# Kernel tuning notes

Measured on AMD Instinct MI355X. Metric: run time of the kernel, lower is better.

## Reference

```python
import jax, jax.numpy as jnp
import numpy as np

N, E, G = 50000, 400000, 2000
H, HEADS, HD = 128, 4, 32


def setup_inputs() -> dict:
    key = jax.random.key(0)
    ks = jax.random.split(key, 16)
    nrm = lambda k, shape, s=0.05: jax.random.normal(k, shape, dtype=jnp.float32) * s
    inp = {}
    inp["x"] = jax.random.normal(ks[0], (N, 39), dtype=jnp.float32)
    inp["edge_index"] = jax.random.randint(ks[1], (2, E), 0, N, dtype=jnp.int32)
    inp["edge_attr"] = jax.random.normal(ks[2], (E, 8), dtype=jnp.float32)
    inp["batch"] = jnp.sort(jax.random.randint(ks[3], (N,), 0, G, dtype=jnp.int32))
    inp["in_W"] = nrm(ks[4], (39, H)); inp["in_b"] = jnp.zeros((H,), jnp.float32)
    inp["in_g"] = jnp.ones((H,), jnp.float32); inp["in_beta"] = jnp.zeros((H,), jnp.float32)
    inp["Wl"] = nrm(ks[5], (3, H, H)); inp["Wr"] = nrm(ks[6], (3, H, H))
    inp["We"] = nrm(ks[7], (3, 8, H)); inp["att"] = nrm(ks[8], (3, HEADS, HD))
    inp["conv_b"] = jnp.zeros((3, H), jnp.float32)
    inp["bn_g"] = jnp.ones((3, H), jnp.float32); inp["bn_b"] = jnp.zeros((3, H), jnp.float32)
    inp["t1_W"] = nrm(ks[9], (3 * H, 256)); inp["t1_b"] = jnp.zeros((256,), jnp.float32)
    inp["t1_g"] = jnp.ones((256,), jnp.float32); inp["t1_beta"] = jnp.zeros((256,), jnp.float32)
    inp["t2_W"] = nrm(ks[10], (256, 128)); inp["t2_b"] = jnp.zeros((128,), jnp.float32)
    inp["t2_g"] = jnp.ones((128,), jnp.float32); inp["t2_beta"] = jnp.zeros((128,), jnp.float32)
    inp["head_W"] = nrm(ks[11], (128, 12)); inp["head_b"] = jnp.zeros((12,), jnp.float32)
    return inp


def _bn(h, g, b):
    # BatchNorm1d in training mode: normalize with batch statistics.
    m = h.mean(0)
    v = ((h - m) ** 2).mean(0)
    return g * (h - m) * jax.lax.rsqrt(v + 1e-5) + b


def reference(x, edge_index, edge_attr, batch, in_W, in_b, in_g, in_beta,
              Wl, Wr, We, att, conv_b, bn_g, bn_b,
              t1_W, t1_b, t1_g, t1_beta, t2_W, t2_b, t2_g, t2_beta,
              head_W, head_b):
    src, dst = edge_index[0], edge_index[1]  # messages flow src -> dst (PyG convention)
    xn = jax.nn.relu(_bn(x @ in_W + in_b, in_g, in_beta))  # [N, H]
    for l in range(3):  # three residual GATv2 layers
        xl = (xn @ Wl[l]).reshape(N, HEADS, HD)  # lin_l (source transform)
        xr = (xn @ Wr[l]).reshape(N, HEADS, HD)  # lin_r (target transform)
        ep = (edge_attr @ We[l]).reshape(E, HEADS, HD)
        m = jax.nn.leaky_relu(xl[src] + xr[dst] + ep, 0.2)  # [E, HEADS, HD]
        alpha = jnp.einsum('ehd,hd->eh', m, att[l])  # [E, HEADS]
        amax = jax.ops.segment_max(alpha, dst, num_segments=N)
        amax = jnp.where(jnp.isfinite(amax), amax, 0.0)  # nodes with no in-edges
        ae = jnp.exp(alpha - amax[dst])
        denom = jax.ops.segment_sum(ae, dst, num_segments=N)
        a = ae / (denom[dst] + 1e-16)  # scatter-softmax over neighborhoods
        agg = jax.ops.segment_sum(xl[src] * a[:, :, None], dst, num_segments=N)
        h = agg.reshape(N, H) + conv_b[l]
        h = jax.nn.elu(_bn(h, bn_g[l], bn_b[l]))
        xn = xn + h
    # 3-way global pooling per graph
    cnt = jax.ops.segment_sum(jnp.ones((N,), jnp.float32), batch, num_segments=G)
    sadd = jax.ops.segment_sum(xn, batch, num_segments=G)
    smean = sadd / jnp.maximum(cnt, 1.0)[:, None]
    smax = jax.ops.segment_max(xn, batch, num_segments=G)
    smax = jnp.where(cnt[:, None] > 0, smax, 0.0)
    xg = jnp.concatenate([smean, smax, sadd], axis=1)  # [G, 3H]
    t = jax.nn.relu(_bn(xg @ t1_W + t1_b, t1_g, t1_beta))
    t = jax.nn.relu(_bn(t @ t2_W + t2_b, t2_g, t2_beta))
    return jax.nn.sigmoid(t @ head_W + head_b)  # [G, 12]
```

## Files before the change

kernel.cpp:

```cpp
#include <hip/hip_runtime.h>
#include <math.h>


constexpr int N_ = 50000;
constexpr int E_ = 400000;
constexpr int G_ = 2000;
constexpr int H_ = 128;
constexpr int IN_ = 39;

typedef __attribute__((ext_vector_type(8))) short bf16x8;
typedef __attribute__((ext_vector_type(4))) float f32x4;

__device__ __forceinline__ unsigned pk_bf16(float a, float b) {
  unsigned ua = __float_as_uint(a);
  unsigned ub = __float_as_uint(b);
  ua = (ua + 0x7fffu + ((ua >> 16) & 1u)) >> 16;
  ub = (ub + 0x7fffu + ((ub >> 16) & 1u)) & 0xffff0000u;
  return ua | ub;
}
__device__ __forceinline__ unsigned short bf16_1(float x) {
  unsigned u = __float_as_uint(x);
  u = (u + 0x7fffu + ((u >> 16) & 1u)) >> 16;
  return (unsigned short)u;
}
__device__ __forceinline__ float up_lo(unsigned u) { return __uint_as_float(u << 16); }
__device__ __forceinline__ float up_hi(unsigned u) { return __uint_as_float(u & 0xffff0000u); }

template <int CTRL>
__device__ __forceinline__ float dpp_radd(float x) {
  int y = __builtin_amdgcn_update_dpp(0, __float_as_int(x), CTRL, 0xF, 0xF, false);
  return x + __int_as_float(y);
}
__device__ __forceinline__ float row_reduce16(float p) {
  p = dpp_radd<0x121>(p);
  p = dpp_radd<0x122>(p);
  p = dpp_radd<0x124>(p);
  p = dpp_radd<0x128>(p);
  return p;
}

__global__ __launch_bounds__(256) void hist_kernel(const int* __restrict__ keys, int n,
                                                   int* __restrict__ cnt) {
  for (int i = blockIdx.x * 256 + threadIdx.x; i < n; i += gridDim.x * 256)
    atomicAdd(&cnt[keys[i]], 1);
}

__global__ __launch_bounds__(1024) void scan_local(const int* __restrict__ in,
                                                   int* __restrict__ outx,
                                                   int* __restrict__ bsum, int n) {
  __shared__ int wsum[16];
  int t = threadIdx.x, lane = t & 63, wid = t >> 6;
  int idx = blockIdx.x * 1024 + t;
  int v = (idx < n) ? in[idx] : 0;
  int x = v;
#pragma unroll
  for (int off = 1; off < 64; off <<= 1) {
    int y = __shfl_up(x, off, 64);
    if (lane >= off) x += y;
  }
  if (lane == 63) wsum[wid] = x;
  __syncthreads();
  if (t == 0) {
    int acc = 0;
#pragma unroll
    for (int w = 0; w < 16; w++) { int tmp = wsum[w]; wsum[w] = acc; acc += tmp; }
    bsum[blockIdx.x] = acc;
  }
  __syncthreads();
  if (idx < n) outx[idx] = wsum[wid] + x - v;
}

__global__ __launch_bounds__(64) void scan_bsum(const int* __restrict__ bsum,
                                                int* __restrict__ boff, int nb) {
  int t = threadIdx.x;
  int v = (t < nb) ? bsum[t] : 0;
  int x = v;
#pragma unroll
  for (int off = 1; off < 64; off <<= 1) {
    int y = __shfl_up(x, off, 64);
    if (t >= off) x += y;
  }
  boff[t] = x - v;
}

__global__ __launch_bounds__(1024) void scan_add(int* __restrict__ eoff,
                                                 const int* __restrict__ boff,
                                                 int* __restrict__ cursor, int n) {
  int idx = blockIdx.x * 1024 + threadIdx.x;
  if (idx < n) {
    int e = eoff[idx] + boff[idx >> 10];
    eoff[idx] = e;
    cursor[idx] = e;
  }
  if (idx == 0) eoff[n] = E_;
}

__global__ __launch_bounds__(256) void goff_from_sorted(const int* __restrict__ batch,
                                                        int* __restrict__ goff) {
  int i = blockIdx.x * 256 + threadIdx.x;
  if (i >= N_) return;
  int bi = batch[i];
  int bp = (i == 0) ? -1 : batch[i - 1];
  for (int g = bp + 1; g <= bi; g++) goff[g] = i;
  if (i == N_ - 1) {
    for (int g = bi + 1; g <= G_; g++) goff[g] = N_;
  }
}

__global__ __launch_bounds__(256) void edge_scatter(const int* __restrict__ ei,
                                                    const float* __restrict__ ea,
                                                    int* __restrict__ cursor,
                                                    int* __restrict__ esrc,
                                                    unsigned* __restrict__ easb) {
  int e = blockIdx.x * 256 + threadIdx.x;
  if (e >= E_) return;
  int src = ei[e];
  int dst = ei[E_ + e];
  int j = atomicAdd(&cursor[dst], 1);
  esrc[j] = src;
  const float4* eav = (const float4*)(ea + (size_t)e * 8);
  float4 a0 = eav[0], a1 = eav[1];
  uint4 o;
  o.x = pk_bf16(a0.x, a0.y);
  o.y = pk_bf16(a0.z, a0.w);
  o.z = pk_bf16(a1.x, a1.y);
  o.w = pk_bf16(a1.z, a1.w);
  ((uint4*)easb)[j] = o;
}

__global__ __launch_bounds__(256) void pack_weights(const float* __restrict__ Wl,
                                                    const float* __restrict__ Wr,
                                                    unsigned short* __restrict__ wpack) {
  int i = blockIdx.x * 256 + threadIdx.x;
  if (i >= 3 * 128 * 256) return;
  int l = i >> 15;
  int rem = i & 32767;
  int k = rem >> 8;
  int n = rem & 255;
  const float* Wsrc = (n < 128) ? (Wl + l * H_ * H_) : (Wr + l * H_ * H_);
  int nn = n & 127;
  wpack[(size_t)l * 32768 + n * 128 + k] = bf16_1(Wsrc[k * H_ + nn]);
}

__global__ __launch_bounds__(256) void in_gemm(const float* __restrict__ x,
                                               const float* __restrict__ W,
                                               const float* __restrict__ b,
                                               float* __restrict__ y,
                                               float* __restrict__ ssum,
                                               float* __restrict__ ssq) {
  __shared__ float xs[32][40];
  __shared__ float s1[256], s2[256];
  int t = threadIdx.x;
  int row0 = blockIdx.x * 32;
  for (int i = t; i < 32 * IN_; i += 256) {
    int r = i / IN_, k = i % IN_;
    int row = row0 + r;
    xs[r][k] = (row < N_) ? x[row * IN_ + k] : 0.f;
  }
  __syncthreads();
  int col = t & 127;
  int half = t >> 7;
  float acc[16];
#pragma unroll
  for (int r = 0; r < 16; r++) acc[r] = 0.f;
  for (int k = 0; k < IN_; k++) {
    float w = W[k * H_ + col];
#pragma unroll
    for (int r = 0; r < 16; r++) acc[r] = fmaf(xs[half * 16 + r][k], w, acc[r]);
  }
  float bb = b[col];
  float a1 = 0.f, a2 = 0.f;
#pragma unroll
  for (int r = 0; r < 16; r++) {
    int row = row0 + half * 16 + r;
    float v = acc[r] + bb;
    if (row < N_) {
      y[row * H_ + col] = v;
      a1 += v;
      a2 = fmaf(v, v, a2);
    }
  }
  s1[t] = a1; s2[t] = a2;
  __syncthreads();
  if (t < 128) {
    atomicAdd(&ssum[t], s1[t] + s1[t + 128]);
    atomicAdd(&ssq[t], s2[t] + s2[t + 128]);
  }
}

template <int MODE>
__global__ __launch_bounds__(256) void gemm_mfma(float* __restrict__ xn,
                                                 const float* __restrict__ buf,
                                                 const float* __restrict__ g,
                                                 const float* __restrict__ beta,
                                                 const float* __restrict__ ssum,
                                                 const float* __restrict__ ssq,
                                                 float rows_inv,
                                                 const unsigned short* __restrict__ wp,
                                                 unsigned* __restrict__ xlb,
                                                 unsigned* __restrict__ xrb) {
  __shared__ char smem[17408 + 20480];
  short (*a_s)[136] = (short(*)[136])smem;
  short (*b_s)[40] = (short(*)[40])(smem + 17408);
  float* t2base = (float*)(smem + 17408);
  int t = threadIdx.x;
  int lane = t & 63, w = t >> 6;
  int quad = lane >> 4, lc = lane & 15;
  int row0 = blockIdx.x * 64;

  {
    int r = t >> 2;
    int row = row0 + r;
    int kb0 = (t & 3) * 32;
    bool valid = row < N_;
    for (int kk = 0; kk < 32; kk += 4) {
      int c = kb0 + kk;
      float4 v = make_float4(0.f, 0.f, 0.f, 0.f);
      if (valid) {
        float4 bv = *(const float4*)&buf[(size_t)row * H_ + c];
        float4 gv = *(const float4*)&g[c];
        float4 be = *(const float4*)&beta[c];
        float4 s1 = *(const float4*)&ssum[c];
        float4 s2 = *(const float4*)&ssq[c];
        float m0 = s1.x * rows_inv, m1 = s1.y * rows_inv, m2 = s1.z * rows_inv, m3 = s1.w * rows_inv;
        float r0 = rsqrtf(s2.x * rows_inv - m0 * m0 + 1e-5f);
        float r1 = rsqrtf(s2.y * rows_inv - m1 * m1 + 1e-5f);
        float r2 = rsqrtf(s2.z * rows_inv - m2 * m2 + 1e-5f);
        float r3 = rsqrtf(s2.w * rows_inv - m3 * m3 + 1e-5f);
        float t0 = gv.x * (bv.x - m0) * r0 + be.x;
        float t1 = gv.y * (bv.y - m1) * r1 + be.y;
        float t2 = gv.z * (bv.z - m2) * r2 + be.z;
        float t3 = gv.w * (bv.w - m3) * r3 + be.w;
        if (MODE == 1) {
          v = make_float4(fmaxf(t0, 0.f), fmaxf(t1, 0.f), fmaxf(t2, 0.f), fmaxf(t3, 0.f));
        } else {
          float4 xo = *(const float4*)&xn[(size_t)row * H_ + c];
          v.x = xo.x + ((t0 > 0.f) ? t0 : (__expf(t0) - 1.f));
          v.y = xo.y + ((t1 > 0.f) ? t1 : (__expf(t1) - 1.f));
          v.z = xo.z + ((t2 > 0.f) ? t2 : (__expf(t2) - 1.f));
          v.w = xo.w + ((t3 > 0.f) ? t3 : (__expf(t3) - 1.f));
        }
        *(float4*)&xn[(size_t)row * H_ + c] = v;
      }
      uint2 pk;
      pk.x = pk_bf16(v.x, v.y);
      pk.y = pk_bf16(v.z, v.w);
      *(uint2*)&a_s[r][c] = pk;
    }
  }

  f32x4 acc[16];
#pragma unroll
  for (int nt = 0; nt < 16; nt++) acc[nt] = (f32x4){0.f, 0.f, 0.f, 0.f};

  for (int kb = 0; kb < 4; kb++) {
    __syncthreads();
    for (int i = t; i < 1024; i += 256) {
      int n = i >> 2;
      int k8 = (i & 3) * 8;
      *(uint4*)&b_s[n][k8] = *(const uint4*)&wp[(size_t)n * 128 + kb * 32 + k8];
    }
    __syncthreads();
    bf16x8 av = *(const bf16x8*)&a_s[w * 16 + lc][kb * 32 + quad * 8];
#pragma unroll
    for (int nt = 0; nt < 16; nt++) {
      bf16x8 bv = *(const bf16x8*)&b_s[nt * 16 + lc][quad * 8];
      acc[nt] = __builtin_amdgcn_mfma_f32_16x16x32_bf16(av, bv, acc[nt], 0, 0, 0);
    }
  }
  __syncthreads();

  float* t2 = t2base + w * 544;
  for (int ntp = 0; ntp < 8; ntp++) {
#pragma unroll
    for (int rr = 0; rr < 4; rr++) {
      t2[(quad * 4 + rr) * 34 + lc] = acc[2 * ntp][rr];
      t2[(quad * 4 + rr) * 34 + 16 + lc] = acc[2 * ntp + 1][rr];
    }
    __asm__ volatile("s_waitcnt lgkmcnt(0)" ::: "memory");
#pragma unroll
    for (int it = 0; it < 4; it++) {
      int item = lane + it * 64;
      int p = item & 15, rowi = item >> 4;
      float v0 = t2[rowi * 34 + 2 * p];
      float v1 = t2[rowi * 34 + 2 * p + 1];
      unsigned u = pk_bf16(v0, v1);
      int colpair = ntp * 16 + p;
      int rowg = row0 + w * 16 + rowi;
      if (rowg < N_) {
        if (colpair < 64) xlb[(size_t)rowg * 64 + colpair] = u;
        else xrb[(size_t)rowg * 64 + colpair - 64] = u;
      }
    }
    __asm__ volatile("s_waitcnt lgkmcnt(0)" ::: "memory");
  }
}

__device__ __forceinline__ float ep8u(const uint4& u, const float* w) {
  float ep = up_lo(u.x) * w[0];
  ep = fmaf(up_hi(u.x), w[1], ep);
  ep = fmaf(up_lo(u.y), w[2], ep);
  ep = fmaf(up_hi(u.y), w[3], ep);
  ep = fmaf(up_lo(u.z), w[4], ep);
  ep = fmaf(up_hi(u.z), w[5], ep);
  ep = fmaf(up_lo(u.w), w[6], ep);
  ep = fmaf(up_hi(u.w), w[7], ep);
  return ep;
}

template <bool MASK>
__device__ __forceinline__ void pack4(int spre, int j, int cnt, int base, int l,
                                      const unsigned* __restrict__ xlb,
                                      const uint4* __restrict__ eas4,
                                      float xr0, float xr1,
                                      const float* w0, const float* w1,
                                      float2 attv,
                                      float& acc0, float& acc1, float& den) {
  int i0 = j;
  int i1 = j + 1, i2 = j + 2, i3 = j + 3;
  if (MASK) {
    i1 = (i1 < cnt) ? i1 : cnt - 1;
    i2 = (i2 < cnt) ? i2 : cnt - 1;
    i3 = (i3 < cnt) ? i3 : cnt - 1;
  }
  int s0 = __builtin_amdgcn_readlane(spre, i0);
  int s1 = __builtin_amdgcn_readlane(spre, i1);
  int s2 = __builtin_amdgcn_readlane(spre, i2);
  int s3 = __builtin_amdgcn_readlane(spre, i3);
  unsigned xu0 = xlb[(size_t)s0 * 64 + l];
  unsigned xu1 = xlb[(size_t)s1 * 64 + l];
  unsigned xu2 = xlb[(size_t)s2 * 64 + l];
  unsigned xu3 = xlb[(size_t)s3 * 64 + l];
  uint4 u0 = eas4[base + i0];
  uint4 u1 = eas4[base + i1];
  uint4 u2 = eas4[base + i2];
  uint4 u3 = eas4[base + i3];
  float x00 = up_lo(xu0), x01 = up_hi(xu0);
  float x10 = up_lo(xu1), x11 = up_hi(xu1);
  float x20 = up_lo(xu2), x21 = up_hi(xu2);
  float x30 = up_lo(xu3), x31 = up_hi(xu3);
  float m00 = x00 + xr0 + ep8u(u0, w0);
  float m01 = x01 + xr1 + ep8u(u0, w1);
  float m10 = x10 + xr0 + ep8u(u1, w0);
  float m11 = x11 + xr1 + ep8u(u1, w1);
  float m20 = x20 + xr0 + ep8u(u2, w0);
  float m21 = x21 + xr1 + ep8u(u2, w1);
  float m30 = x30 + xr0 + ep8u(u3, w0);
  float m31 = x31 + xr1 + ep8u(u3, w1);
  m00 = (m00 > 0.f) ? m00 : 0.2f * m00;
  m01 = (m01 > 0.f) ? m01 : 0.2f * m01;
  m10 = (m10 > 0.f) ? m10 : 0.2f * m10;
  m11 = (m11 > 0.f) ? m11 : 0.2f * m11;
  m20 = (m20 > 0.f) ? m20 : 0.2f * m20;
  m21 = (m21 > 0.f) ? m21 : 0.2f * m21;
  m30 = (m30 > 0.f) ? m30 : 0.2f * m30;
  m31 = (m31 > 0.f) ? m31 : 0.2f * m31;
  float p0 = fmaf(m00, attv.x, m01 * attv.y);
  float p1 = fmaf(m10, attv.x, m11 * attv.y);
  float p2 = fmaf(m20, attv.x, m21 * attv.y);
  float p3 = fmaf(m30, attv.x, m31 * attv.y);
  p0 = row_reduce16(p0);
  p1 = row_reduce16(p1);
  p2 = row_reduce16(p2);
  p3 = row_reduce16(p3);
  float e0v = __expf(p0), e1v = __expf(p1), e2v = __expf(p2), e3v = __expf(p3);
  if (MASK) {
    if (j + 1 >= cnt) e1v = 0.f;
    if (j + 2 >= cnt) e2v = 0.f;
    if (j + 3 >= cnt) e3v = 0.f;
  }
  acc0 = fmaf(e0v, x00, acc0); acc1 = fmaf(e0v, x01, acc1);
  acc0 = fmaf(e1v, x10, acc0); acc1 = fmaf(e1v, x11, acc1);
  acc0 = fmaf(e2v, x20, acc0); acc1 = fmaf(e2v, x21, acc1);
  acc0 = fmaf(e3v, x30, acc0); acc1 = fmaf(e3v, x31, acc1);
  den += (e0v + e1v) + (e2v + e3v);
}

__device__ __forceinline__ void solo_node(int e0, int e1, int l,
                                          const int* __restrict__ esrc,
                                          const unsigned* __restrict__ xlb,
                                          const uint4* __restrict__ eas4,
                                          float xr0, float xr1,
                                          const float* w0, const float* w1,
                                          float2 attv,
                                          float& acc0, float& acc1, float& den) {
  for (int base = e0; base < e1; base += 64) {
    int cnt = min(64, e1 - base);
    int spre = (base + l < e1) ? esrc[base + l] : 0;
    int j = 0;
    for (; j + 4 <= cnt; j += 4)
      pack4<false>(spre, j, cnt, base, l, xlb, eas4, xr0, xr1, w0, w1, attv, acc0, acc1, den);
    if (j < cnt)
      pack4<true>(spre, j, cnt, base, l, xlb, eas4, xr0, xr1, w0, w1, attv, acc0, acc1, den);
  }
}

__global__ __launch_bounds__(256) void agg_csr(const int* __restrict__ eoff,
                                               const int* __restrict__ esrc,
                                               const unsigned* __restrict__ easb,
                                               const float* __restrict__ Wel,
                                               const float* __restrict__ attl,
                                               const unsigned* __restrict__ xlb,
                                               const unsigned* __restrict__ xrb,
                                               const float* __restrict__ cb,
                                               float* __restrict__ buf,
                                               float* __restrict__ ssum,
                                               float* __restrict__ ssq) {
  __shared__ float sA[256], sB[256], sC[256], sD[256];
  __shared__ uint4 eaLds[4][64];
  int t = threadIdx.x;
  int l = t & 63;
  int sub = t >> 6;
  int c0 = l * 2;
  uint4* eaW = &eaLds[sub][0];
  float w0[8], w1[8];
#pragma unroll
  for (int k = 0; k < 8; k++) {
    float2 wv = *(const float2*)&Wel[k * H_ + c0];
    w0[k] = wv.x; w1[k] = wv.y;
  }
  float2 attv = *(const float2*)&attl[c0];
  float2 cbv = *(const float2*)&cb[c0];
  const uint4* eas4 = (const uint4*)easb;
  float a1_0 = 0.f, a1_1 = 0.f, a2_0 = 0.f, a2_1 = 0.f;

  for (int pi = blockIdx.x * 4 + sub; pi < N_ / 2; pi += gridDim.x * 4) {
    int nA = 2 * pi, nB = nA + 1;
    int e0A = eoff[nA], e1A = eoff[nA + 1], e1B = eoff[nA + 2];
    unsigned xruA = xrb[(size_t)nA * 64 + l];
    unsigned xruB = xrb[(size_t)nB * 64 + l];
    int cE = e1B - e0A;
    float hA0, hA1, hB0, hB1;
    if (cE <= 64) {
      int cA = e1A - e0A, cB = e1B - e1A;
      if (l < cE) eaW[l] = eas4[e0A + l];
      int spre = (l < cE) ? esrc[e0A + l] : 0;
      __asm__ volatile("s_waitcnt lgkmcnt(0)" ::: "memory");
      int nPA = (cA + 3) >> 2;
      int nP = nPA + ((cB + 3) >> 2);
      float accA0 = 0.f, accA1 = 0.f, denA = 0.f;
      float accB0 = 0.f, accB1 = 0.f, denB = 0.f;
      unsigned xu0 = 0, xu1 = 0, xu2 = 0, xu3 = 0;
      int i0 = 0, i1 = 0, i2 = 0, i3 = 0;
      if (nP > 0) {
        bool isA = 0 < nPA;
        int off = isA ? 0 : cA;
        int cnt = isA ? cA : cB;
        int lim = off + cnt - 1;
        i0 = off;
        i1 = min(off + 1, lim); i2 = min(off + 2, lim); i3 = min(off + 3, lim);
        xu0 = xlb[(size_t)__builtin_amdgcn_readlane(spre, i0) * 64 + l];
        xu1 = xlb[(size_t)__builtin_amdgcn_readlane(spre, i1) * 64 + l];
        xu2 = xlb[(size_t)__builtin_amdgcn_readlane(spre, i2) * 64 + l];
        xu3 = xlb[(size_t)__builtin_amdgcn_readlane(spre, i3) * 64 + l];
      }
      for (int k = 0; k < nP; k++) {
        unsigned t0 = xu0, t1 = xu1, t2 = xu2, t3 = xu3;
        int ci0 = i0, ci1 = i1, ci2 = i2, ci3 = i3;
        bool isA = k < nPA;
        int j = isA ? 4 * k : 4 * (k - nPA);
        int cnt = isA ? cA : cB;
        if (k + 1 < nP) {
          bool pA = (k + 1) < nPA;
          int off2 = pA ? 0 : cA;
          int cnt2 = pA ? cA : cB;
          int j2 = pA ? 4 * (k + 1) : 4 * (k + 1 - nPA);
          int b2 = off2 + j2;
          int lim2 = off2 + cnt2 - 1;
          i0 = b2;
          i1 = min(b2 + 1, lim2); i2 = min(b2 + 2, lim2); i3 = min(b2 + 3, lim2);
          xu0 = xlb[(size_t)__builtin_amdgcn_readlane(spre, i0) * 64 + l];
          xu1 = xlb[(size_t)__builtin_amdgcn_readlane(spre, i1) * 64 + l];
          xu2 = xlb[(size_t)__builtin_amdgcn_readlane(spre, i2) * 64 + l];
          xu3 = xlb[(size_t)__builtin_amdgcn_readlane(spre, i3) * 64 + l];
        }
        uint4 u0 = eaW[ci0], u1 = eaW[ci1], u2 = eaW[ci2], u3 = eaW[ci3];
        unsigned xrp = isA ? xruA : xruB;
        float xr0 = up_lo(xrp), xr1 = up_hi(xrp);
        float x00 = up_lo(t0), x01 = up_hi(t0);
        float x10 = up_lo(t1), x11 = up_hi(t1);
        float x20 = up_lo(t2), x21 = up_hi(t2);
        float x30 = up_lo(t3), x31 = up_hi(t3);
        float m00 = x00 + xr0 + ep8u(u0, w0);
        float m01 = x01 + xr1 + ep8u(u0, w1);
        float m10 = x10 + xr0 + ep8u(u1, w0);
        float m11 = x11 + xr1 + ep8u(u1, w1);
        float m20 = x20 + xr0 + ep8u(u2, w0);
        float m21 = x21 + xr1 + ep8u(u2, w1);
        float m30 = x30 + xr0 + ep8u(u3, w0);
        float m31 = x31 + xr1 + ep8u(u3, w1);
        m00 = (m00 > 0.f) ? m00 : 0.2f * m00;
        m01 = (m01 > 0.f) ? m01 : 0.2f * m01;
        m10 = (m10 > 0.f) ? m10 : 0.2f * m10;
        m11 = (m11 > 0.f) ? m11 : 0.2f * m11;
        m20 = (m20 > 0.f) ? m20 : 0.2f * m20;
        m21 = (m21 > 0.f) ? m21 : 0.2f * m21;
        m30 = (m30 > 0.f) ? m30 : 0.2f * m30;
        m31 = (m31 > 0.f) ? m31 : 0.2f * m31;
        float p0 = fmaf(m00, attv.x, m01 * attv.y);
        float p1 = fmaf(m10, attv.x, m11 * attv.y);
        float p2 = fmaf(m20, attv.x, m21 * attv.y);
        float p3 = fmaf(m30, attv.x, m31 * attv.y);
        p0 = row_reduce16(p0);
        p1 = row_reduce16(p1);
        p2 = row_reduce16(p2);
        p3 = row_reduce16(p3);
        float e0v = __expf(p0), e1v = __expf(p1), e2v = __expf(p2), e3v = __expf(p3);
        if (j + 1 >= cnt) e1v = 0.f;
        if (j + 2 >= cnt) e2v = 0.f;
        if (j + 3 >= cnt) e3v = 0.f;
        if (isA) {
          accA0 = fmaf(e0v, x00, accA0); accA1 = fmaf(e0v, x01, accA1);
          accA0 = fmaf(e1v, x10, accA0); accA1 = fmaf(e1v, x11, accA1);
          accA0 = fmaf(e2v, x20, accA0); accA1 = fmaf(e2v, x21, accA1);
          accA0 = fmaf(e3v, x30, accA0); accA1 = fmaf(e3v, x31, accA1);
          denA += (e0v + e1v) + (e2v + e3v);
        } else {
          accB0 = fmaf(e0v, x00, accB0); accB1 = fmaf(e0v, x01, accB1);
          accB0 = fmaf(e1v, x10, accB0); accB1 = fmaf(e1v, x11, accB1);
          accB0 = fmaf(e2v, x20, accB0); accB1 = fmaf(e2v, x21, accB1);
          accB0 = fmaf(e3v, x30, accB0); accB1 = fmaf(e3v, x31, accB1);
          denB += (e0v + e1v) + (e2v + e3v);
        }
      }
      float invA = 1.f / (denA + 1e-16f);
      float invB = 1.f / (denB + 1e-16f);
      hA0 = accA0 * invA + cbv.x; hA1 = accA1 * invA + cbv.y;
      hB0 = accB0 * invB + cbv.x; hB1 = accB1 * invB + cbv.y;
    } else {
      float accA0 = 0.f, accA1 = 0.f, denA = 0.f;
      float accB0 = 0.f, accB1 = 0.f, denB = 0.f;
      solo_node(e0A, e1A, l, esrc, xlb, eas4, up_lo(xruA), up_hi(xruA),
                w0, w1, attv, accA0, accA1, denA);
      solo_node(e1A, e1B, l, esrc, xlb, eas4, up_lo(xruB), up_hi(xruB),
                w0, w1, attv, accB0, accB1, denB);
      float invA = 1.f / (denA + 1e-16f);
      float invB = 1.f / (denB + 1e-16f);
      hA0 = accA0 * invA + cbv.x; hA1 = accA1 * invA + cbv.y;
      hB0 = accB0 * invB + cbv.x; hB1 = accB1 * invB + cbv.y;
    }
    *(float2*)&buf[(size_t)nA * H_ + c0] = make_float2(hA0, hA1);
    *(float2*)&buf[(size_t)nB * H_ + c0] = make_float2(hB0, hB1);
    a1_0 += hA0 + hB0; a1_1 += hA1 + hB1;
    a2_0 = fmaf(hA0, hA0, a2_0); a2_0 = fmaf(hB0, hB0, a2_0);
    a2_1 = fmaf(hA1, hA1, a2_1); a2_1 = fmaf(hB1, hB1, a2_1);
  }
  sA[t] = a1_0; sB[t] = a1_1; sC[t] = a2_0; sD[t] = a2_1;
  __syncthreads();
  if (t < 64) {
    float r1 = sA[t] + sA[t + 64] + sA[t + 128] + sA[t + 192];
    float r2 = sB[t] + sB[t + 64] + sB[t + 128] + sB[t + 192];
    float r3 = sC[t] + sC[t + 64] + sC[t + 128] + sC[t + 192];
    float r4 = sD[t] + sD[t + 64] + sD[t + 128] + sD[t + 192];
    atomicAdd(&ssum[2 * t], r1);
    atomicAdd(&ssum[2 * t + 1], r2);
    atomicAdd(&ssq[2 * t], r3);
    atomicAdd(&ssq[2 * t + 1], r4);
  }
}

__global__ __launch_bounds__(256) void apply_bn_relu(const float* __restrict__ y,
                                                     float* __restrict__ out,
                                                     const float* __restrict__ g,
                                                     const float* __restrict__ beta,
                                                     const float* __restrict__ ssum,
                                                     const float* __restrict__ ssq,
                                                     float rows_inv,
                                                     long total, int cmask) {
  long i = (long)blockIdx.x * 256 + threadIdx.x;
  if (i >= total) return;
  int c = (int)i & cmask;
  float m = ssum[c] * rows_inv;
  float rs = rsqrtf(ssq[c] * rows_inv - m * m + 1e-5f);
  float v = g[c] * (y[i] - m) * rs + beta[c];
  out[i] = fmaxf(v, 0.f);
}

__global__ __launch_bounds__(128) void pool_residual(const int* __restrict__ goff,
                                                     const float* __restrict__ xn,
                                                     const float* __restrict__ buf,
                                                     const float* __restrict__ g,
                                                     const float* __restrict__ beta,
                                                     const float* __restrict__ ssum,
                                                     const float* __restrict__ ssq,
                                                     float rows_inv,
                                                     float* __restrict__ xg) {
  int gr = blockIdx.x;
  int t = threadIdx.x;
  int n0 = goff[gr], n1 = goff[gr + 1];
  float mm = ssum[t] * rows_inv;
  float rr = rsqrtf(ssq[t] * rows_inv - mm * mm + 1e-5f);
  float gg = g[t], bb = beta[t];
  float s = 0.f, mx = -INFINITY;
  for (int n = n0; n < n1; n++) {
    float w = gg * (buf[(size_t)n * H_ + t] - mm) * rr + bb;
    w = (w > 0.f) ? w : (__expf(w) - 1.f);
    float v = xn[(size_t)n * H_ + t] + w;
    s += v;
    mx = fmaxf(mx, v);
  }
  float c = (float)(n1 - n0);
  xg[gr * 384 + t] = s / fmaxf(c, 1.f);
  xg[gr * 384 + 128 + t] = (c > 0.f) ? mx : 0.f;
  xg[gr * 384 + 256 + t] = s;
}

template <int K, int COLS>
__global__ void mlp_gemm(const float* __restrict__ A, const float* __restrict__ W,
                         const float* __restrict__ b, float* __restrict__ Y, int rows,
                         float* __restrict__ ssum, float* __restrict__ ssq) {
  __shared__ float xs[8][K];
  int t = threadIdx.x;
  int row0 = blockIdx.x * 8;
  for (int i = t; i < 8 * K; i += COLS) {
    int r = i / K, k = i % K;
    int row = row0 + r;
    xs[r][k] = (row < rows) ? A[row * K + k] : 0.f;
  }
  __syncthreads();
  float acc[8];
#pragma unroll
  for (int r = 0; r < 8; r++) acc[r] = 0.f;
  for (int k = 0; k < K; k++) {
    float w = W[k * COLS + t];
#pragma unroll
    for (int r = 0; r < 8; r++) acc[r] = fmaf(xs[r][k], w, acc[r]);
  }
  float bb = b[t];
  float a1 = 0.f, a2 = 0.f;
#pragma unroll
  for (int r = 0; r < 8; r++) {
    int row = row0 + r;
    if (row < rows) {
      float v = acc[r] + bb;
      Y[row * COLS + t] = v;
      a1 += v;
      a2 = fmaf(v, v, a2);
    }
  }
  atomicAdd(&ssum[t], a1);
  atomicAdd(&ssq[t], a2);
}

__global__ __launch_bounds__(64) void head_kernel(const float* __restrict__ u,
                                                  const float* __restrict__ W,
                                                  const float* __restrict__ b,
                                                  float* __restrict__ out) {
  __shared__ float row[128];
  int g = blockIdx.x;
  int t = threadIdx.x;
  row[t] = u[g * 128 + t];
  row[t + 64] = u[g * 128 + 64 + t];
  __syncthreads();
  if (t < 12) {
    float acc = b[t];
    for (int k = 0; k < 128; k++) acc = fmaf(row[k], W[k * 12 + t], acc);
    out[g * 12 + t] = 1.f / (1.f + expf(-acc));
  }
}

extern "C" void kernel_launch(void* const* d_in, const int* in_sizes, int n_in, void* d_out,
                              int out_size, void* d_ws, size_t ws_size, hipStream_t stream) {
  (void)in_sizes; (void)n_in; (void)out_size; (void)ws_size;
  const float* x       = (const float*)d_in[0];
  const int*   ei      = (const int*)d_in[1];
  const float* ea      = (const float*)d_in[2];
  const int*   batch   = (const int*)d_in[3];
  const float* in_W    = (const float*)d_in[4];
  const float* in_b    = (const float*)d_in[5];
  const float* in_g    = (const float*)d_in[6];
  const float* in_beta = (const float*)d_in[7];
  const float* Wl      = (const float*)d_in[8];
  const float* Wr      = (const float*)d_in[9];
  const float* We      = (const float*)d_in[10];
  const float* att     = (const float*)d_in[11];
  const float* conv_b  = (const float*)d_in[12];
  const float* bn_g    = (const float*)d_in[13];
  const float* bn_b    = (const float*)d_in[14];
  const float* t1_W    = (const float*)d_in[15];
  const float* t1_b    = (const float*)d_in[16];
  const float* t1_g    = (const float*)d_in[17];
  const float* t1_beta = (const float*)d_in[18];
  const float* t2_W    = (const float*)d_in[19];
  const float* t2_b    = (const float*)d_in[20];
  const float* t2_g    = (const float*)d_in[21];
  const float* t2_beta = (const float*)d_in[22];
  const float* head_W  = (const float*)d_in[23];
  const float* head_b  = (const float*)d_in[24];
  float* out = (float*)d_out;

  float* p = (float*)d_ws;
  float* xn    = p; p += N_ * H_;
  float* buf   = p; p += N_ * H_;
  float* sstat = p; p += 6 * 512;
  float* xg    = p; p += G_ * 384;
  float* u1    = p; p += G_ * 256;
  float* u2    = p; p += G_ * 128;
  unsigned* up = (unsigned*)p;
  unsigned* xlb  = up; up += (size_t)N_ * 64;
  unsigned* xrb  = up; up += (size_t)N_ * 64;
  unsigned* easb = up; up += (size_t)E_ * 4;
  unsigned short* wpack = (unsigned short*)up; up += 3 * 32768 / 2;
  int* ip = (int*)up;
  int* deg    = ip; ip += N_;
  int* eoff   = ip; ip += N_ + 1;
  int* cursor = ip; ip += N_;
  int* goff   = ip; ip += G_ + 1;
  int* esrc   = ip; ip += E_;
  int* bsum   = ip; ip += 64;
  int* boff   = ip; ip += 64;

#define SSUM(s) (sstat + (s) * 512)
#define SSQ(s)  (sstat + (s) * 512 + 256)

  hipMemsetAsync(deg, 0, (size_t)N_ * sizeof(int), stream);
  hipMemsetAsync(sstat, 0, 6 * 512 * sizeof(float), stream);
  hist_kernel<<<1024, 256, 0, stream>>>(ei + E_, E_, deg);
  scan_local<<<49, 1024, 0, stream>>>(deg, eoff, bsum, N_);
  scan_bsum<<<1, 64, 0, stream>>>(bsum, boff, 49);
  scan_add<<<49, 1024, 0, stream>>>(eoff, boff, cursor, N_);
  edge_scatter<<<(E_ + 255) / 256, 256, 0, stream>>>(ei, ea, cursor, esrc, easb);
  goff_from_sorted<<<(N_ + 255) / 256, 256, 0, stream>>>(batch, goff);
  pack_weights<<<384, 256, 0, stream>>>(Wl, Wr, wpack);

  in_gemm<<<(N_ + 31) / 32, 256, 0, stream>>>(x, in_W, in_b, buf, SSUM(0), SSQ(0));

  const float rnInv = 1.f / N_;
  for (int l = 0; l < 3; l++) {
    if (l == 0) {
      gemm_mfma<1><<<782, 256, 0, stream>>>(xn, buf, in_g, in_beta, SSUM(0), SSQ(0), rnInv,
                                            wpack + (size_t)l * 32768, xlb, xrb);
    } else {
      gemm_mfma<2><<<782, 256, 0, stream>>>(xn, buf, bn_g + (l - 1) * H_, bn_b + (l - 1) * H_,
                                            SSUM(l), SSQ(l), rnInv,
                                            wpack + (size_t)l * 32768, xlb, xrb);
    }
    agg_csr<<<2048, 256, 0, stream>>>(eoff, esrc, easb, We + l * 8 * H_, att + l * H_,
                                      xlb, xrb, conv_b + l * H_, buf, SSUM(l + 1), SSQ(l + 1));
  }

  pool_residual<<<G_, 128, 0, stream>>>(goff, xn, buf, bn_g + 2 * H_, bn_b + 2 * H_,
                                        SSUM(3), SSQ(3), rnInv, xg);

  const float rgInv = 1.f / G_;
  mlp_gemm<384, 256><<<G_ / 8, 256, 0, stream>>>(xg, t1_W, t1_b, u1, G_, SSUM(4), SSQ(4));
  apply_bn_relu<<<(G_ * 256 + 255) / 256, 256, 0, stream>>>(u1, u1, t1_g, t1_beta,
                                                            SSUM(4), SSQ(4), rgInv,
                                                            (long)G_ * 256, 255);

  mlp_gemm<256, 128><<<G_ / 8, 128, 0, stream>>>(u1, t2_W, t2_b, u2, G_, SSUM(5), SSQ(5));
  apply_bn_relu<<<(G_ * 128 + 255) / 256, 256, 0, stream>>>(u2, u2, t2_g, t2_beta,
                                                            SSUM(5), SSQ(5), rgInv,
                                                            (long)G_ * 128, 127);

  head_kernel<<<G_, 64, 0, stream>>>(u2, head_W, head_b, out);
#undef SSUM
#undef SSQ
}
```

Baseline: 841.4 us.

## Merge setup kernels, use single-pass decoupled scan, fold MLP BN into consumers

Four independent setup kernels (degree histogram, graph offsets, weight packing, input GEMM) become one launch that dispatches by block index. The three-kernel prefix scan becomes a single-pass chained scan in which each block spins on its predecessor's published prefix. The two MLP BatchNorm+ReLU passes are folded into the next GEMM's load stage and into the head kernel, and the two memsets are merged into one. The aim is fewer launches and less global traffic. The chained scan relies on all 49 blocks making forward progress, and the BN parameters are recomputed per element in the consumers.

```diff
diff --git a/kernel.cpp b/kernel.cpp
--- a/kernel.cpp
+++ b/kernel.cpp
@@ -7,6 +7,11 @@
 constexpr int G_ = 2000;
 constexpr int H_ = 128;
 constexpr int IN_ = 39;
+
+constexpr int HIST_B = 1024;
+constexpr int GOFF_B = (N_ + 255) / 256;
+constexpr int PACK_B = 384;
+constexpr int INGEMM_B = (N_ + 31) / 32;
 
 typedef __attribute__((ext_vector_type(8))) short bf16x8;
 typedef __attribute__((ext_vector_type(4))) float f32x4;
@@ -39,19 +44,101 @@
   return p;
 }
 
-__global__ __launch_bounds__(256) void hist_kernel(const int* __restrict__ keys, int n,
-                                                   int* __restrict__ cnt) {
-  for (int i = blockIdx.x * 256 + threadIdx.x; i < n; i += gridDim.x * 256)
-    atomicAdd(&cnt[keys[i]], 1);
-}
-
-__global__ __launch_bounds__(1024) void scan_local(const int* __restrict__ in,
-                                                   int* __restrict__ outx,
-                                                   int* __restrict__ bsum, int n) {
+__global__ __launch_bounds__(256) void prep_kernel(const int* __restrict__ ei,
+                                                   const int* __restrict__ batch,
+                                                   const float* __restrict__ Wl,
+                                                   const float* __restrict__ Wr,
+                                                   const float* __restrict__ x,
+                                                   const float* __restrict__ in_W,
+                                                   const float* __restrict__ in_b,
+                                                   int* __restrict__ deg,
+                                                   int* __restrict__ goff,
+                                                   unsigned short* __restrict__ wpack,
+                                                   float* __restrict__ y,
+                                                   float* __restrict__ ssum,
+                                                   float* __restrict__ ssq) {
+  int b = blockIdx.x;
+  int t = threadIdx.x;
+  if (b < HIST_B) {
+    for (int i = b * 256 + t; i < E_; i += HIST_B * 256)
+      atomicAdd(&deg[ei[E_ + i]], 1);
+    return;
+  }
+  b -= HIST_B;
+  if (b < GOFF_B) {
+    int i = b * 256 + t;
+    if (i >= N_) return;
+    int bi = batch[i];
+    int bp = (i == 0) ? -1 : batch[i - 1];
+    for (int g = bp + 1; g <= bi; g++) goff[g] = i;
+    if (i == N_ - 1) {
+      for (int g = bi + 1; g <= G_; g++) goff[g] = N_;
+    }
+    return;
+  }
+  b -= GOFF_B;
+  if (b < PACK_B) {
+    int i = b * 256 + t;
+    if (i >= 3 * 128 * 256) return;
+    int l = i >> 15;
+    int rem = i & 32767;
+    int k = rem >> 8;
+    int n = rem & 255;
+    const float* Wsrc = (n < 128) ? (Wl + l * H_ * H_) : (Wr + l * H_ * H_);
+    int nn = n & 127;
+    wpack[(size_t)l * 32768 + n * 128 + k] = bf16_1(Wsrc[k * H_ + nn]);
+    return;
+  }
+  b -= PACK_B;
+  __shared__ float xs[32][40];
+  __shared__ float s1[256], s2[256];
+  int row0 = b * 32;
+  for (int i = t; i < 32 * IN_; i += 256) {
+    int r = i / IN_, k = i % IN_;
+    int row = row0 + r;
+    xs[r][k] = (row < N_) ? x[row * IN_ + k] : 0.f;
+  }
+  __syncthreads();
+  int col = t & 127;
+  int half = t >> 7;
+  float acc[16];
+#pragma unroll
+  for (int r = 0; r < 16; r++) acc[r] = 0.f;
+  for (int k = 0; k < IN_; k++) {
+    float w = in_W[k * H_ + col];
+#pragma unroll
+    for (int r = 0; r < 16; r++) acc[r] = fmaf(xs[half * 16 + r][k], w, acc[r]);
+  }
+  float bb = in_b[col];
+  float a1 = 0.f, a2 = 0.f;
+#pragma unroll
+  for (int r = 0; r < 16; r++) {
+    int row = row0 + half * 16 + r;
+    float v = acc[r] + bb;
+    if (row < N_) {
+      y[row * H_ + col] = v;
+      a1 += v;
+      a2 = fmaf(v, v, a2);
+    }
+  }
+  s1[t] = a1; s2[t] = a2;
+  __syncthreads();
+  if (t < 128) {
+    atomicAdd(&ssum[t], s1[t] + s1[t + 128]);
+    atomicAdd(&ssq[t], s2[t] + s2[t + 128]);
+  }
+}
+
+__global__ __launch_bounds__(1024) void scan_onepass(const int* __restrict__ deg,
+                                                     int* __restrict__ eoff,
+                                                     int* __restrict__ cursor,
+                                                     int* __restrict__ pref, int n) {
   __shared__ int wsum[16];
+  __shared__ int sbase;
   int t = threadIdx.x, lane = t & 63, wid = t >> 6;
-  int idx = blockIdx.x * 1024 + t;
-  int v = (idx < n) ? in[idx] : 0;
+  int b = blockIdx.x;
+  int idx = b * 1024 + t;
+  int v = (idx < n) ? deg[idx] : 0;
   int x = v;
 #pragma unroll
   for (int off = 1; off < 64; off <<= 1) {
@@ -64,46 +151,21 @@
     int acc = 0;
 #pragma unroll
     for (int w = 0; w < 16; w++) { int tmp = wsum[w]; wsum[w] = acc; acc += tmp; }
-    bsum[blockIdx.x] = acc;
-  }
-  __syncthreads();
-  if (idx < n) outx[idx] = wsum[wid] + x - v;
-}
-
-__global__ __launch_bounds__(64) void scan_bsum(const int* __restrict__ bsum,
-                                                int* __restrict__ boff, int nb) {
-  int t = threadIdx.x;
-  int v = (t < nb) ? bsum[t] : 0;
-  int x = v;
-#pragma unroll
-  for (int off = 1; off < 64; off <<= 1) {
-    int y = __shfl_up(x, off, 64);
-    if (t >= off) x += y;
-  }
-  boff[t] = x - v;
-}
-
-__global__ __launch_bounds__(1024) void scan_add(int* __restrict__ eoff,
-                                                 const int* __restrict__ boff,
-                                                 int* __restrict__ cursor, int n) {
-  int idx = blockIdx.x * 1024 + threadIdx.x;
+    int prev = 0;
+    if (b > 0) {
+      int got;
+      do { got = atomicAdd(&pref[b - 1], 0); } while (got == 0);
+      prev = got - 1;
+    }
+    atomicExch(&pref[b], prev + acc + 1);
+    sbase = prev;
+  }
+  __syncthreads();
   if (idx < n) {
-    int e = eoff[idx] + boff[idx >> 10];
+    int e = sbase + wsum[wid] + x - v;
     eoff[idx] = e;
     cursor[idx] = e;
-  }
-  if (idx == 0) eoff[n] = E_;
-}
-
-__global__ __launch_bounds__(256) void goff_from_sorted(const int* __restrict__ batch,
-                                                        int* __restrict__ goff) {
-  int i = blockIdx.x * 256 + threadIdx.x;
-  if (i >= N_) return;
-  int bi = batch[i];
-  int bp = (i == 0) ? -1 : batch[i - 1];
-  for (int g = bp + 1; g <= bi; g++) goff[g] = i;
-  if (i == N_ - 1) {
-    for (int g = bi + 1; g <= G_; g++) goff[g] = N_;
+    if (idx == n - 1) eoff[n] = E_;
   }
 }
 
@@ -126,66 +188,6 @@
   o.z = pk_bf16(a1.x, a1.y);
   o.w = pk_bf16(a1.z, a1.w);
   ((uint4*)easb)[j] = o;
-}
-
-__global__ __launch_bounds__(256) void pack_weights(const float* __restrict__ Wl,
-                                                    const float* __restrict__ Wr,
-                                                    unsigned short* __restrict__ wpack) {
-  int i = blockIdx.x * 256 + threadIdx.x;
-  if (i >= 3 * 128 * 256) return;
-  int l = i >> 15;
-  int rem = i & 32767;
-  int k = rem >> 8;
-  int n = rem & 255;
-  const float* Wsrc = (n < 128) ? (Wl + l * H_ * H_) : (Wr + l * H_ * H_);
-  int nn = n & 127;
-  wpack[(size_t)l * 32768 + n * 128 + k] = bf16_1(Wsrc[k * H_ + nn]);
-}
-
-__global__ __launch_bounds__(256) void in_gemm(const float* __restrict__ x,
-                                               const float* __restrict__ W,
-                                               const float* __restrict__ b,
-                                               float* __restrict__ y,
-                                               float* __restrict__ ssum,
-                                               float* __restrict__ ssq) {
-  __shared__ float xs[32][40];
-  __shared__ float s1[256], s2[256];
-  int t = threadIdx.x;
-  int row0 = blockIdx.x * 32;
-  for (int i = t; i < 32 * IN_; i += 256) {
-    int r = i / IN_, k = i % IN_;
-    int row = row0 + r;
-    xs[r][k] = (row < N_) ? x[row * IN_ + k] : 0.f;
-  }
-  __syncthreads();
-  int col = t & 127;
-  int half = t >> 7;
-  float acc[16];
-#pragma unroll
-  for (int r = 0; r < 16; r++) acc[r] = 0.f;
-  for (int k = 0; k < IN_; k++) {
-    float w = W[k * H_ + col];
-#pragma unroll
-    for (int r = 0; r < 16; r++) acc[r] = fmaf(xs[half * 16 + r][k], w, acc[r]);
-  }
-  float bb = b[col];
-  float a1 = 0.f, a2 = 0.f;
-#pragma unroll
-  for (int r = 0; r < 16; r++) {
-    int row = row0 + half * 16 + r;
-    float v = acc[r] + bb;
-    if (row < N_) {
-      y[row * H_ + col] = v;
-      a1 += v;
-      a2 = fmaf(v, v, a2);
-    }
-  }
-  s1[t] = a1; s2[t] = a2;
-  __syncthreads();
-  if (t < 128) {
-    atomicAdd(&ssum[t], s1[t] + s1[t + 128]);
-    atomicAdd(&ssq[t], s2[t] + s2[t + 128]);
-  }
 }
 
 template <int MODE>
@@ -559,23 +561,6 @@
   }
 }
 
-__global__ __launch_bounds__(256) void apply_bn_relu(const float* __restrict__ y,
-                                                     float* __restrict__ out,
-                                                     const float* __restrict__ g,
-                                                     const float* __restrict__ beta,
-                                                     const float* __restrict__ ssum,
-                                                     const float* __restrict__ ssq,
-                                                     float rows_inv,
-                                                     long total, int cmask) {
-  long i = (long)blockIdx.x * 256 + threadIdx.x;
-  if (i >= total) return;
-  int c = (int)i & cmask;
-  float m = ssum[c] * rows_inv;
-  float rs = rsqrtf(ssq[c] * rows_inv - m * m + 1e-5f);
-  float v = g[c] * (y[i] - m) * rs + beta[c];
-  out[i] = fmaxf(v, 0.f);
-}
-
 __global__ __launch_bounds__(128) void pool_residual(const int* __restrict__ goff,
                                                      const float* __restrict__ xn,
                                                      const float* __restrict__ buf,
@@ -605,24 +590,23 @@
   xg[gr * 384 + 256 + t] = s;
 }
 
-template <int K, int COLS>
-__global__ void mlp_gemm(const float* __restrict__ A, const float* __restrict__ W,
-                         const float* __restrict__ b, float* __restrict__ Y, int rows,
-                         float* __restrict__ ssum, float* __restrict__ ssq) {
-  __shared__ float xs[8][K];
+__global__ void mlp_gemm1(const float* __restrict__ A, const float* __restrict__ W,
+                          const float* __restrict__ b, float* __restrict__ Y, int rows,
+                          float* __restrict__ ssum, float* __restrict__ ssq) {
+  __shared__ float xs[8][384];
   int t = threadIdx.x;
   int row0 = blockIdx.x * 8;
-  for (int i = t; i < 8 * K; i += COLS) {
-    int r = i / K, k = i % K;
+  for (int i = t; i < 8 * 384; i += 256) {
+    int r = i / 384, k = i % 384;
     int row = row0 + r;
-    xs[r][k] = (row < rows) ? A[row * K + k] : 0.f;
+    xs[r][k] = (row < rows) ? A[row * 384 + k] : 0.f;
   }
   __syncthreads();
   float acc[8];
 #pragma unroll
   for (int r = 0; r < 8; r++) acc[r] = 0.f;
-  for (int k = 0; k < K; k++) {
-    float w = W[k * COLS + t];
+  for (int k = 0; k < 384; k++) {
+    float w = W[k * 256 + t];
 #pragma unroll
     for (int r = 0; r < 8; r++) acc[r] = fmaf(xs[r][k], w, acc[r]);
   }
@@ -633,7 +617,7 @@
     int row = row0 + r;
     if (row < rows) {
       float v = acc[r] + bb;
-      Y[row * COLS + t] = v;
+      Y[row * 256 + t] = v;
       a1 += v;
       a2 = fmaf(v, v, a2);
     }
@@ -642,20 +626,77 @@
   atomicAdd(&ssq[t], a2);
 }
 
+__global__ void mlp_gemm2(const float* __restrict__ A,
+                          const float* __restrict__ g4, const float* __restrict__ be4,
+                          const float* __restrict__ s4, const float* __restrict__ q4,
+                          float rinv,
+                          const float* __restrict__ W, const float* __restrict__ b,
+                          float* __restrict__ Y, int rows,
+                          float* __restrict__ ssum, float* __restrict__ ssq) {
+  __shared__ float xs[8][256];
+  int t = threadIdx.x;
+  int row0 = blockIdx.x * 8;
+  for (int i = t; i < 8 * 256; i += 128) {
+    int r = i >> 8, k = i & 255;
+    int row = row0 + r;
+    float v = 0.f;
+    if (row < rows) {
+      float m = s4[k] * rinv;
+      float rs = rsqrtf(q4[k] * rinv - m * m + 1e-5f);
+      v = fmaxf(g4[k] * (A[row * 256 + k] - m) * rs + be4[k], 0.f);
+    }
+    xs[r][k] = v;
+  }
+  __syncthreads();
+  float acc[8];
+#pragma unroll
+  for (int r = 0; r < 8; r++) acc[r] = 0.f;
+  for (int k = 0; k < 256; k++) {
+    float w = W[k * 128 + t];
+#pragma unroll
+    for (int r = 0; r < 8; r++) acc[r] = fmaf(xs[r][k], w, acc[r]);
+  }
+  float bb = b[t];
+  float a1 = 0.f, a2 = 0.f;
+#pragma unroll
+  for (int r = 0; r < 8; r++) {
+    int row = row0 + r;
+    if (row < rows) {
+      float v = acc[r] + bb;
+      Y[row * 128 + t] = v;
+      a1 += v;
+      a2 = fmaf(v, v, a2);
+    }
+  }
+  atomicAdd(&ssum[t], a1);
+  atomicAdd(&ssq[t], a2);
+}
+
 __global__ __launch_bounds__(64) void head_kernel(const float* __restrict__ u,
+                                                  const float* __restrict__ g5,
+                                                  const float* __restrict__ be5,
+                                                  const float* __restrict__ s5,
+                                                  const float* __restrict__ q5,
+                                                  float rinv,
                                                   const float* __restrict__ W,
                                                   const float* __restrict__ b,
                                                   float* __restrict__ out) {
   __shared__ float row[128];
-  int g = blockIdx.x;
+  int gblk = blockIdx.x;
   int t = threadIdx.x;
-  row[t] = u[g * 128 + t];
-  row[t + 64] = u[g * 128 + 64 + t];
+#pragma unroll
+  for (int h = 0; h < 2; h++) {
+    int c = t + h * 64;
+    float m = s5[c] * rinv;
+    float rs = rsqrtf(q5[c] * rinv - m * m + 1e-5f);
+    float v = g5[c] * (u[gblk * 128 + c] - m) * rs + be5[c];
+    row[c] = fmaxf(v, 0.f);
+  }
   __syncthreads();
   if (t < 12) {
     float acc = b[t];
     for (int k = 0; k < 128; k++) acc = fmaf(row[k], W[k * 12 + t], acc);
-    out[g * 12 + t] = 1.f / (1.f + expf(-acc));
+    out[gblk * 12 + t] = 1.f / (1.f + expf(-acc));
   }
 }
 
@@ -692,38 +733,33 @@
   float* p = (float*)d_ws;
   float* xn    = p; p += N_ * H_;
   float* buf   = p; p += N_ * H_;
-  float* sstat = p; p += 6 * 512;
   float* xg    = p; p += G_ * 384;
   float* u1    = p; p += G_ * 256;
   float* u2    = p; p += G_ * 128;
-  unsigned* up = (unsigned*)p;
+  float* sstat = p; p += 6 * 512;
+  int* ip = (int*)p;
+  int* deg    = ip; ip += N_;
+  int* pref   = ip; ip += 64;
+  int* eoff   = ip; ip += N_ + 1;
+  int* cursor = ip; ip += N_;
+  int* goff   = ip; ip += G_ + 1;
+  int* esrc   = ip; ip += E_;
+  unsigned* up = (unsigned*)ip;
   unsigned* xlb  = up; up += (size_t)N_ * 64;
   unsigned* xrb  = up; up += (size_t)N_ * 64;
   unsigned* easb = up; up += (size_t)E_ * 4;
   unsigned short* wpack = (unsigned short*)up; up += 3 * 32768 / 2;
-  int* ip = (int*)up;
-  int* deg    = ip; ip += N_;
-  int* eoff   = ip; ip += N_ + 1;
-  int* cursor = ip; ip += N_;
-  int* goff   = ip; ip += G_ + 1;
-  int* esrc   = ip; ip += E_;
-  int* bsum   = ip; ip += 64;
-  int* boff   = ip; ip += 64;
 
 #define SSUM(s) (sstat + (s) * 512)
 #define SSQ(s)  (sstat + (s) * 512 + 256)
 
-  hipMemsetAsync(deg, 0, (size_t)N_ * sizeof(int), stream);
-  hipMemsetAsync(sstat, 0, 6 * 512 * sizeof(float), stream);
-  hist_kernel<<<1024, 256, 0, stream>>>(ei + E_, E_, deg);
-  scan_local<<<49, 1024, 0, stream>>>(deg, eoff, bsum, N_);
-  scan_bsum<<<1, 64, 0, stream>>>(bsum, boff, 49);
-  scan_add<<<49, 1024, 0, stream>>>(eoff, boff, cursor, N_);
+  hipMemsetAsync(sstat, 0, (size_t)(6 * 512 + N_ + 64) * sizeof(int), stream);
+
+  prep_kernel<<<HIST_B + GOFF_B + PACK_B + INGEMM_B, 256, 0, stream>>>(
+      ei, batch, Wl, Wr, x, in_W, in_b, deg, goff, wpack, buf, SSUM(0), SSQ(0));
+
+  scan_onepass<<<49, 1024, 0, stream>>>(deg, eoff, cursor, pref, N_);
   edge_scatter<<<(E_ + 255) / 256, 256, 0, stream>>>(ei, ea, cursor, esrc, easb);
-  goff_from_sorted<<<(N_ + 255) / 256, 256, 0, stream>>>(batch, goff);
-  pack_weights<<<384, 256, 0, stream>>>(Wl, Wr, wpack);
-
-  in_gemm<<<(N_ + 31) / 32, 256, 0, stream>>>(x, in_W, in_b, buf, SSUM(0), SSQ(0));
 
   const float rnInv = 1.f / N_;
   for (int l = 0; l < 3; l++) {
@@ -743,17 +779,11 @@
                                         SSUM(3), SSQ(3), rnInv, xg);
 
   const float rgInv = 1.f / G_;
-  mlp_gemm<384, 256><<<G_ / 8, 256, 0, stream>>>(xg, t1_W, t1_b, u1, G_, SSUM(4), SSQ(4));
-  apply_bn_relu<<<(G_ * 256 + 255) / 256, 256, 0, stream>>>(u1, u1, t1_g, t1_beta,
-                                                            SSUM(4), SSQ(4), rgInv,
-                                                            (long)G_ * 256, 255);
-
-  mlp_gemm<256, 128><<<G_ / 8, 128, 0, stream>>>(u1, t2_W, t2_b, u2, G_, SSUM(5), SSQ(5));
-  apply_bn_relu<<<(G_ * 128 + 255) / 256, 256, 0, stream>>>(u2, u2, t2_g, t2_beta,
-                                                            SSUM(5), SSQ(5), rgInv,
-                                                            (long)G_ * 128, 127);
-
-  head_kernel<<<G_, 64, 0, stream>>>(u2, head_W, head_b, out);
+  mlp_gemm1<<<G_ / 8, 256, 0, stream>>>(xg, t1_W, t1_b, u1, G_, SSUM(4), SSQ(4));
+  mlp_gemm2<<<G_ / 8, 128, 0, stream>>>(u1, t1_g, t1_beta, SSUM(4), SSQ(4), rgInv,
+                                        t2_W, t2_b, u2, G_, SSUM(5), SSQ(5));
+  head_kernel<<<G_, 64, 0, stream>>>(u2, t2_g, t2_beta, SSUM(5), SSQ(5), rgInv,
+                                     head_W, head_b, out);
 #undef SSUM
 #undef SSQ
 }
```

Result: no change. 841.1 us (-0.0%).
